# Performance work log

Measured on AMD Instinct MI355X. Metric: run time of the kernel, lower is better.

## Reference

```python
import jax, jax.numpy as jnp
import numpy as np
from jax import lax

T, B, IN, H, L, C = 1024, 2048, 2, 20, 6, 2


def setup_inputs() -> dict:
    key = jax.random.key(0)
    ks = jax.random.split(key, 8)
    s = 1.0 / np.sqrt(H)  # PyTorch RNN init scale (uniform bound); use scaled normals
    return {
        "x": jax.random.normal(ks[0], (T, B, IN), jnp.float32),
        "W_ih0": jax.random.normal(ks[1], (H, IN), jnp.float32) * s,
        "W_ih": jax.random.normal(ks[2], (L - 1, H, H), jnp.float32) * s,
        "W_hh": jax.random.normal(ks[3], (L, H, H), jnp.float32) * s,
        "b_ih": jax.random.normal(ks[4], (L, H), jnp.float32) * s,
        "b_hh": jax.random.normal(ks[5], (L, H), jnp.float32) * s,
        "fc_w": jax.random.normal(ks[6], (C, H), jnp.float32) * s,
        "fc_b": jax.random.normal(ks[7], (C,), jnp.float32) * s,
    }


def _rnn_layer(x, Wih, Whh, bih, bhh):
    # x: [T, B, in_dim]; h_t = relu(x_t @ Wih^T + b_ih + h_{t-1} @ Whh^T + b_hh)
    xb = jnp.einsum('tbi,hi->tbh', x, Wih) + (bih + bhh)  # precompute input projection
    h0 = jnp.zeros((x.shape[1], Whh.shape[0]), x.dtype)

    def step(h, xt):
        h = jax.nn.relu(xt + h @ Whh.T)
        return h, h

    _, out = lax.scan(step, h0, xb)
    return out  # [T, B, H]


def reference(x, W_ih0, W_ih, W_hh, b_ih, b_hh, fc_w, fc_b):
    out = _rnn_layer(x, W_ih0, W_hh[0], b_ih[0], b_hh[0])
    for l in range(1, L):
        out = _rnn_layer(out, W_ih[l - 1], W_hh[l], b_ih[l], b_hh[l])
    logits = jnp.einsum('tbh,ch->tbc', out, fc_w) + fc_b
    return jax.nn.log_softmax(logits, axis=2)
```

## Files before the change

### kernel.cpp

```cpp
#include <hip/hip_runtime.h>
#include <math.h>


#define TT 1024
#define BB 2048
#define HH 20
#define LL 6
#define SLOTW 40
#define BUFW  (8 * SLOTW)
#define NSTEPS (TT + LL)

#define WS_WI   0
#define WS_BIAS 2400

struct SteadyT { static constexpr bool value = true;  };
struct EdgeT   { static constexpr bool value = false; };

__global__ void stage_ws(const float* __restrict__ Wih0,
                         const float* __restrict__ Wih,
                         const float* __restrict__ bih,
                         const float* __restrict__ bhh,
                         const float* __restrict__ fcb,
                         float* __restrict__ ws) {
    const int i = threadIdx.x + blockIdx.x * blockDim.x;
    if (i < 2400) {
        const int l = i / 400, r = i % 400, j = r / 20, k = r % 20;
        float v;
        if (l == 0) v = (k < 2) ? Wih0[j * 2 + k] : 0.f;
        else        v = Wih[(l - 1) * 400 + r];
        ws[WS_WI + i] = v;
    }
    if (i < 122) {
        const int role = i >> 1, c = i & 1;
        float v;
        if (role < 60) {
            const int l = role / 10, j = 2 * (role % 10) + c;
            v = bih[l * HH + j] + bhh[l * HH + j];
        } else {
            v = fcb[c];
        }
        ws[WS_BIAS + i] = v;
    }
}

__global__ void logsm(float* __restrict__ o) {
    const size_t n = (size_t)TT * BB;
    float2* p = (float2*)o;
    for (size_t idx = (size_t)blockIdx.x * blockDim.x + threadIdx.x; idx < n;
         idx += (size_t)gridDim.x * blockDim.x) {
        float2 v = p[idx];
        const float mx  = fmaxf(v.x, v.y);
        const float lse = mx + __logf(__expf(v.x - mx) + __expf(v.y - mx));
        p[idx] = make_float2(v.x - lse, v.y - lse);
    }
}

__global__ __attribute__((amdgpu_flat_work_group_size(64, 64), amdgpu_waves_per_eu(2, 2)))
void rnn_fused(const float* __restrict__ x,
               const float* __restrict__ Whh,
               const float* __restrict__ fcw,
               const float* __restrict__ ws,
               float* __restrict__ out)
{
    __shared__ __align__(16) float As[2 * BUFW];

    const int lane = threadIdx.x;
    const int b = ((blockIdx.x & 7) << 8) | (blockIdx.x >> 3);

    const int  role = (lane < 60) ? lane : 60;
    const int  l    = role / 10;
    const int  j    = 2 * (role % 10);
    const bool head = (role == 60);

    const float4* pwh = (const float4*)(head ? Whh : (Whh + (l * HH + j) * HH));
    const float4* pwi = (const float4*)(head ? fcw : (ws + WS_WI + (l * HH + j) * HH));
    const float2  bt  = *(const float2*)(ws + WS_BIAS + 2 * role);

    float4 whA[5], whB[5], wiA[5], wiB[5];
#pragma unroll
    for (int q = 0; q < 5; ++q) {
        whA[q] = pwh[q];
        whB[q] = pwh[5 + q];
        wiA[q] = pwi[q];
        wiB[q] = pwi[5 + q];
    }

    for (int i = lane; i < 2 * BUFW; i += 64) As[i] = 0.f;

    const float2* xp = (const float2*)x;
    float2 xh = make_float2(0.f, 0.f);
    if (lane == 61) *(float2*)&As[0] = xp[b];
    if (lane >= 61) xh = xp[(size_t)(lane - 60) * BB + b];

    const int ioff = l * SLOTW;
    const int hoff = (l + 1) * SLOTW;

    const int rdc = (lane >= 61) ? (lane - 61) : 0;
    float2*       oph  = (float2*)out + b - (ptrdiff_t)LL * BB;
    const float2* xq   = xp + (size_t)(rdc + 4) * BB + b;
    const float2* xend = xp + (size_t)(TT - 1) * BB + b;

    auto step = [&](int s, int ph, const float* rb, float* wb, auto sc) {
        constexpr bool STEADY = decltype(sc)::value;
        const float4* hp = (const float4*)(rb + hoff);
        const float4* ip = (const float4*)(rb + ioff);

        float ah0 = 0.f, ah1 = 0.f;
        float ai0 = bt.x, ai1 = bt.y;
#pragma unroll
        for (int q = 0; q < 5; ++q) {
            const float4 h4 = hp[q];
            const float4 i4 = ip[q];
            ah0 = fmaf(whA[q].x, h4.x, ah0); ah0 = fmaf(whA[q].y, h4.y, ah0);
            ah0 = fmaf(whA[q].z, h4.z, ah0); ah0 = fmaf(whA[q].w, h4.w, ah0);
            ah1 = fmaf(whB[q].x, h4.x, ah1); ah1 = fmaf(whB[q].y, h4.y, ah1);
            ah1 = fmaf(whB[q].z, h4.z, ah1); ah1 = fmaf(whB[q].w, h4.w, ah1);
            ai0 = fmaf(wiA[q].x, i4.x, ai0); ai0 = fmaf(wiA[q].y, i4.y, ai0);
            ai0 = fmaf(wiA[q].z, i4.z, ai0); ai0 = fmaf(wiA[q].w, i4.w, ai0);
            ai1 = fmaf(wiB[q].x, i4.x, ai1); ai1 = fmaf(wiB[q].y, i4.y, ai1);
            ai1 = fmaf(wiB[q].z, i4.z, ai1); ai1 = fmaf(wiB[q].w, i4.w, ai1);
        }
        const float a0 = ah0 + ai0;
        const float a1 = ah1 + ai1;

        if (role < 60) {
            if (STEADY || (unsigned)(s - l) < TT) {
                float2 r;
                r.x = fmaxf(a0, 0.f);
                r.y = fmaxf(a1, 0.f);
                *(float2*)(wb + hoff + j) = r;
            }
        } else if (lane == 60) {
            if (STEADY || s >= LL) *oph = make_float2(a0, a1);
            oph += BB;
        } else {
            if (rdc == ph) {
                if (STEADY || s + 1 < TT) *(float2*)wb = xh;
                if (STEADY)              xh = *xq;
                else if (xq <= xend)     xh = *xq;
                xq += 3 * (size_t)BB;
            }
        }
        __builtin_amdgcn_sched_barrier(0);
    };

    float* const buf0 = As;
    float* const buf1 = As + BUFW;

    step(0, 0, buf0, buf1, EdgeT{}); step(1, 1, buf1, buf0, EdgeT{});
    step(2, 2, buf0, buf1, EdgeT{}); step(3, 0, buf1, buf0, EdgeT{});
    step(4, 1, buf0, buf1, EdgeT{}); step(5, 2, buf1, buf0, EdgeT{});

#pragma unroll 1
    for (int it = 0; it < 169; ++it) {
        step(0, 0, buf0, buf1, SteadyT{}); step(0, 1, buf1, buf0, SteadyT{});
        step(0, 2, buf0, buf1, SteadyT{}); step(0, 0, buf1, buf0, SteadyT{});
        step(0, 1, buf0, buf1, SteadyT{}); step(0, 2, buf1, buf0, SteadyT{});
    }

    step(1020, 0, buf0, buf1, EdgeT{}); step(1021, 1, buf1, buf0, EdgeT{});
    step(1022, 2, buf0, buf1, EdgeT{}); step(1023, 0, buf1, buf0, EdgeT{});
    step(1024, 1, buf0, buf1, EdgeT{}); step(1025, 2, buf1, buf0, EdgeT{});
    step(1026, 0, buf0, buf1, EdgeT{}); step(1027, 1, buf1, buf0, EdgeT{});
    step(1028, 2, buf0, buf1, EdgeT{}); step(1029, 0, buf1, buf0, EdgeT{});
}

extern "C" void kernel_launch(void* const* d_in, const int* in_sizes, int n_in,
                              void* d_out, int out_size, void* d_ws, size_t ws_size,
                              hipStream_t stream) {
    const float* x    = (const float*)d_in[0];
    const float* Wih0 = (const float*)d_in[1];
    const float* Wih  = (const float*)d_in[2];
    const float* Whh  = (const float*)d_in[3];
    const float* bih  = (const float*)d_in[4];
    const float* bhh  = (const float*)d_in[5];
    const float* fcw  = (const float*)d_in[6];
    const float* fcb  = (const float*)d_in[7];
    float* out = (float*)d_out;
    float* ws  = (float*)d_ws;

    stage_ws<<<dim3(3), dim3(1024), 0, stream>>>(Wih0, Wih, bih, bhh, fcb, ws);
    rnn_fused<<<dim3(BB), dim3(64), 0, stream>>>(x, Whh, fcw, ws, out);
    logsm<<<dim3(2048), dim3(256), 0, stream>>>(out);
}
```

Baseline: 426.7 us.

## Software-pipeline LDS reads across steps with doubled layer lag in wavefront RNN

Restructures the fused layer-wavefront RNN so each micro-step reads its input-slot vector one step ahead and reloads its own hidden state right after writing it. Layer skew goes from 1 to 2 steps (lag2 = 2*l), which lets the input projection use values loaded a step earlier and hides LDS latency behind the FMAs. Total steps grow from 1030 to 1036 and register pressure rises from the extra prefetch registers. The point is to take LDS read latency off the serial dependency chain.

```diff
diff --git a/kernel.cpp b/kernel.cpp
--- a/kernel.cpp
+++ b/kernel.cpp
@@ -8,13 +8,12 @@
 #define LL 6
 #define SLOTW 40
 #define BUFW  (8 * SLOTW)
-#define NSTEPS (TT + LL)
+#define XS 0
 
 #define WS_WI   0
 #define WS_BIAS 2400
 
-struct SteadyT { static constexpr bool value = true;  };
-struct EdgeT   { static constexpr bool value = false; };
+typedef float f4 __attribute__((ext_vector_type(4)));
 
 __global__ void stage_ws(const float* __restrict__ Wih0,
                          const float* __restrict__ Wih,
@@ -55,6 +54,51 @@
     }
 }
 
+
+#define MAC4(acc, W, Q) do {                                       \
+    acc = fmaf((W).x, (Q).x, acc); acc = fmaf((W).y, (Q).y, acc);  \
+    acc = fmaf((W).z, (Q).z, acc); acc = fmaf((W).w, (Q).w, acc); } while (0)
+
+#define MICRO(M_, C0,C1,C2,C3,C4, N0,N1,N2,N3,N4, ST_) do {                        \
+    float* const wb_ = (((M_) & 1) ? bufB : bufA);                                 \
+    const float* const rb_ = (((M_) & 1) ? bufA : bufB);                           \
+    { const f4* jp_ = (const f4*)(rb_ + ioff);                                     \
+      N0 = jp_[0]; N1 = jp_[1]; N2 = jp_[2]; N3 = jp_[3]; N4 = jp_[4]; }           \
+    float ai0 = bt.x, ai1 = bt.y, ah0 = 0.f, ah1 = 0.f;                            \
+    MAC4(ai0, wiA0, C0); MAC4(ai1, wiB0, C0);                                      \
+    MAC4(ai0, wiA1, C1); MAC4(ai1, wiB1, C1);                                      \
+    MAC4(ai0, wiA2, C2); MAC4(ai1, wiB2, C2);                                      \
+    MAC4(ai0, wiA3, C3); MAC4(ai1, wiB3, C3);                                      \
+    MAC4(ai0, wiA4, C4); MAC4(ai1, wiB4, C4);                                      \
+    MAC4(ah0, whA0, rq0); MAC4(ah1, whB0, rq0);                                    \
+    MAC4(ah0, whA1, rq1); MAC4(ah1, whB1, rq1);                                    \
+    MAC4(ah0, whA2, rq2); MAC4(ah1, whB2, rq2);                                    \
+    MAC4(ah0, whA3, rq3); MAC4(ah1, whB3, rq3);                                    \
+    MAC4(ah0, whA4, rq4); MAC4(ah1, whB4, rq4);                                    \
+    const float a0 = ah0 + ai0;                                                    \
+    const float a1 = ah1 + ai1;                                                    \
+    if (lane < 60) {                                                               \
+        if ((ST_) || (unsigned)((M_) - lag2) < TT)                                 \
+            *(float2*)(wb_ + hoff + j) = make_float2(fmaxf(a0, 0.f), fmaxf(a1, 0.f)); \
+    } else if (lane == 60) {                                                       \
+        if ((ST_) || (unsigned)((M_) - 12) < TT) *oph = make_float2(a0, a1);       \
+        oph += BB;                                                                 \
+    } else {                                                                       \
+        if (rdc == ((M_) % 3)) {                                                   \
+            if ((ST_) || (M_) + 2 < TT) *(float2*)(wb_ + XS) = xh;                 \
+            if ((ST_)) xh = *xq; else if (xq <= xend) xh = *xq;                    \
+            xq += 3 * (size_t)BB;                                                  \
+        }                                                                          \
+    }                                                                              \
+    { const f4* hp_ = (const f4*)(wb_ + hoff);                                     \
+      rq0 = hp_[0]; rq1 = hp_[1]; rq2 = hp_[2]; rq3 = hp_[3]; rq4 = hp_[4]; }      \
+    __builtin_amdgcn_sched_barrier(0);                                             \
+} while (0)
+
+#define MPAIR(M_, ST_)                                                             \
+    MICRO((M_),     iq0,iq1,iq2,iq3,iq4, jq0,jq1,jq2,jq3,jq4, ST_);                \
+    MICRO((M_) + 1, jq0,jq1,jq2,jq3,jq4, iq0,iq1,iq2,iq3,iq4, ST_)
+
 __global__ __attribute__((amdgpu_flat_work_group_size(64, 64), amdgpu_waves_per_eu(2, 2)))
 void rnn_fused(const float* __restrict__ x,
                const float* __restrict__ Whh,
@@ -71,98 +115,53 @@
     const int  l    = role / 10;
     const int  j    = 2 * (role % 10);
     const bool head = (role == 60);
+    const int  lag2 = 2 * l;
 
-    const float4* pwh = (const float4*)(head ? Whh : (Whh + (l * HH + j) * HH));
-    const float4* pwi = (const float4*)(head ? fcw : (ws + WS_WI + (l * HH + j) * HH));
-    const float2  bt  = *(const float2*)(ws + WS_BIAS + 2 * role);
+    const f4* pwh = (const f4*)(head ? Whh : (Whh + (l * HH + j) * HH));
+    const f4* pwi = (const f4*)(head ? fcw : (ws + WS_WI + (l * HH + j) * HH));
+    const float2 bt = *(const float2*)(ws + WS_BIAS + 2 * role);
 
-    float4 whA[5], whB[5], wiA[5], wiB[5];
-#pragma unroll
-    for (int q = 0; q < 5; ++q) {
-        whA[q] = pwh[q];
-        whB[q] = pwh[5 + q];
-        wiA[q] = pwi[q];
-        wiB[q] = pwi[5 + q];
-    }
-
-    for (int i = lane; i < 2 * BUFW; i += 64) As[i] = 0.f;
-
-    const float2* xp = (const float2*)x;
-    float2 xh = make_float2(0.f, 0.f);
-    if (lane == 61) *(float2*)&As[0] = xp[b];
-    if (lane >= 61) xh = xp[(size_t)(lane - 60) * BB + b];
+    f4 whA0 = pwh[0], whA1 = pwh[1], whA2 = pwh[2], whA3 = pwh[3], whA4 = pwh[4];
+    f4 whB0 = pwh[5], whB1 = pwh[6], whB2 = pwh[7], whB3 = pwh[8], whB4 = pwh[9];
+    f4 wiA0 = pwi[0], wiA1 = pwi[1], wiA2 = pwi[2], wiA3 = pwi[3], wiA4 = pwi[4];
+    f4 wiB0 = pwi[5], wiB1 = pwi[6], wiB2 = pwi[7], wiB3 = pwi[8], wiB4 = pwi[9];
 
     const int ioff = l * SLOTW;
     const int hoff = (l + 1) * SLOTW;
 
+    float* const bufA = As;
+    float* const bufB = As + BUFW;
+
+    for (int i = lane; i < 2 * BUFW; i += 64) As[i] = 0.f;
+    const float2* xp = (const float2*)x;
+    float2 xh = make_float2(0.f, 0.f);
+    if (lane == 61) *(float2*)(bufA + XS) = xp[b];
+    if (lane == 62) *(float2*)(bufB + XS) = xp[(size_t)BB + b];
+    if (lane >= 61) xh = xp[(size_t)(lane - 61 + 2) * BB + b];
+
     const int rdc = (lane >= 61) ? (lane - 61) : 0;
-    float2*       oph  = (float2*)out + b - (ptrdiff_t)LL * BB;
-    const float2* xq   = xp + (size_t)(rdc + 4) * BB + b;
+    const float2* xq   = xp + (size_t)(rdc + 5) * BB + b;
     const float2* xend = xp + (size_t)(TT - 1) * BB + b;
+    float2* oph = (float2*)out + b - (ptrdiff_t)12 * BB;
 
-    auto step = [&](int s, int ph, const float* rb, float* wb, auto sc) {
-        constexpr bool STEADY = decltype(sc)::value;
-        const float4* hp = (const float4*)(rb + hoff);
-        const float4* ip = (const float4*)(rb + ioff);
+    f4 iq0, iq1, iq2, iq3, iq4, jq0, jq1, jq2, jq3, jq4;
+    f4 rq0, rq1, rq2, rq3, rq4;
+    { const f4* ip_ = (const f4*)(bufA + ioff);
+      iq0 = ip_[0]; iq1 = ip_[1]; iq2 = ip_[2]; iq3 = ip_[3]; iq4 = ip_[4]; }
+    { const f4* hp_ = (const f4*)(bufB + hoff);
+      rq0 = hp_[0]; rq1 = hp_[1]; rq2 = hp_[2]; rq3 = hp_[3]; rq4 = hp_[4]; }
 
-        float ah0 = 0.f, ah1 = 0.f;
-        float ai0 = bt.x, ai1 = bt.y;
-#pragma unroll
-        for (int q = 0; q < 5; ++q) {
-            const float4 h4 = hp[q];
-            const float4 i4 = ip[q];
-            ah0 = fmaf(whA[q].x, h4.x, ah0); ah0 = fmaf(whA[q].y, h4.y, ah0);
-            ah0 = fmaf(whA[q].z, h4.z, ah0); ah0 = fmaf(whA[q].w, h4.w, ah0);
-            ah1 = fmaf(whB[q].x, h4.x, ah1); ah1 = fmaf(whB[q].y, h4.y, ah1);
-            ah1 = fmaf(whB[q].z, h4.z, ah1); ah1 = fmaf(whB[q].w, h4.w, ah1);
-            ai0 = fmaf(wiA[q].x, i4.x, ai0); ai0 = fmaf(wiA[q].y, i4.y, ai0);
-            ai0 = fmaf(wiA[q].z, i4.z, ai0); ai0 = fmaf(wiA[q].w, i4.w, ai0);
-            ai1 = fmaf(wiB[q].x, i4.x, ai1); ai1 = fmaf(wiB[q].y, i4.y, ai1);
-            ai1 = fmaf(wiB[q].z, i4.z, ai1); ai1 = fmaf(wiB[q].w, i4.w, ai1);
-        }
-        const float a0 = ah0 + ai0;
-        const float a1 = ah1 + ai1;
-
-        if (role < 60) {
-            if (STEADY || (unsigned)(s - l) < TT) {
-                float2 r;
-                r.x = fmaxf(a0, 0.f);
-                r.y = fmaxf(a1, 0.f);
-                *(float2*)(wb + hoff + j) = r;
-            }
-        } else if (lane == 60) {
-            if (STEADY || s >= LL) *oph = make_float2(a0, a1);
-            oph += BB;
-        } else {
-            if (rdc == ph) {
-                if (STEADY || s + 1 < TT) *(float2*)wb = xh;
-                if (STEADY)              xh = *xq;
-                else if (xq <= xend)     xh = *xq;
-                xq += 3 * (size_t)BB;
-            }
-        }
-        __builtin_amdgcn_sched_barrier(0);
-    };
-
-    float* const buf0 = As;
-    float* const buf1 = As + BUFW;
-
-    step(0, 0, buf0, buf1, EdgeT{}); step(1, 1, buf1, buf0, EdgeT{});
-    step(2, 2, buf0, buf1, EdgeT{}); step(3, 0, buf1, buf0, EdgeT{});
-    step(4, 1, buf0, buf1, EdgeT{}); step(5, 2, buf1, buf0, EdgeT{});
+    MPAIR(0, 0);  MPAIR(2, 0);  MPAIR(4, 0);
+    MPAIR(6, 0);  MPAIR(8, 0);  MPAIR(10, 0);
 
 #pragma unroll 1
-    for (int it = 0; it < 169; ++it) {
-        step(0, 0, buf0, buf1, SteadyT{}); step(0, 1, buf1, buf0, SteadyT{});
-        step(0, 2, buf0, buf1, SteadyT{}); step(0, 0, buf1, buf0, SteadyT{});
-        step(0, 1, buf0, buf1, SteadyT{}); step(0, 2, buf1, buf0, SteadyT{});
+    for (int it = 0; it < 167; ++it) {
+        MPAIR(12, 1); MPAIR(14, 1); MPAIR(16, 1);
     }
 
-    step(1020, 0, buf0, buf1, EdgeT{}); step(1021, 1, buf1, buf0, EdgeT{});
-    step(1022, 2, buf0, buf1, EdgeT{}); step(1023, 0, buf1, buf0, EdgeT{});
-    step(1024, 1, buf0, buf1, EdgeT{}); step(1025, 2, buf1, buf0, EdgeT{});
-    step(1026, 0, buf0, buf1, EdgeT{}); step(1027, 1, buf1, buf0, EdgeT{});
-    step(1028, 2, buf0, buf1, EdgeT{}); step(1029, 0, buf1, buf0, EdgeT{});
+    MPAIR(1014, 0); MPAIR(1016, 0); MPAIR(1018, 0); MPAIR(1020, 0);
+    MPAIR(1022, 0); MPAIR(1024, 0); MPAIR(1026, 0); MPAIR(1028, 0);
+    MPAIR(1030, 0); MPAIR(1032, 0); MPAIR(1034, 0);
 }
 
 extern "C" void kernel_launch(void* const* d_in, const int* in_sizes, int n_in,
```

Result: no change. 429.6 us (+0.7%).
